# Kernel tuning notes

Measured on AMD Instinct MI355X. Metric: run time of the kernel, lower is better.

The kernel has to match this reference:

```python
import jax, jax.numpy as jnp
import numpy as np

N, E, IN, HID, HEADS, OUT = 50000, 800000, 2, 64, 4, 64


def setup_inputs() -> dict:
    key = jax.random.key(0)
    ks = jax.random.split(key, 16)
    g = lambda k, s: (jax.random.normal(k, s, dtype=jnp.float32) * 0.1)
    return {
        "x": jax.random.normal(ks[0], (N, IN), dtype=jnp.float32),
        # GraphConv(in->hid): lin_rel (with bias) on aggregated neighbors + lin_root on x
        "W_rel": g(ks[1], (IN, HID)), "b_rel": jnp.zeros((HID,), jnp.float32), "W_root": g(ks[2], (IN, HID)),
        # GATConv(hid -> hid, heads=4, concat)
        "W1": g(ks[3], (HID, HEADS * HID)), "a_src1": g(ks[4], (HEADS, HID)), "a_dst1": g(ks[5], (HEADS, HID)), "b1": jnp.zeros((HEADS * HID,), jnp.float32),
        # GATConv(hid*heads -> hid, heads=4, concat)
        "W2": g(ks[6], (HID * HEADS, HEADS * HID)), "a_src2": g(ks[7], (HEADS, HID)), "a_dst2": g(ks[8], (HEADS, HID)), "b2": jnp.zeros((HEADS * HID,), jnp.float32),
        # GATConv(hid*heads -> out, heads=1, concat=False)
        "W3": g(ks[9], (HID * HEADS, OUT)), "a_src3": g(ks[10], (1, OUT)), "a_dst3": g(ks[11], (1, OUT)), "b3": jnp.zeros((OUT,), jnp.float32),
        "edge_index": jax.random.randint(ks[12], (2, E), 0, N, dtype=jnp.int64),
    }


def graph_conv(x, src, dst, W_rel, b_rel, W_root, n):
    # out_i = (sum_{j->i} x_j) @ W_rel + b_rel + x_i @ W_root
    agg = jax.ops.segment_sum(x[src], dst, num_segments=n)
    return agg @ W_rel + b_rel + x @ W_root


def gat_conv(x, src, dst, W, a_s, a_d, b, heads, oc, concat):
    # src/dst already include self-loops (PyG add_self_loops=True default)
    n = x.shape[0]
    h = (x @ W).reshape(n, heads, oc)                      # [n, heads, oc]
    al_s = jnp.einsum("nhc,hc->nh", h, a_s)               # alpha_src per node
    al_d = jnp.einsum("nhc,hc->nh", h, a_d)               # alpha_dst per node
    e = jax.nn.leaky_relu(al_s[src] + al_d[dst], 0.2)     # [E, heads]
    m = jax.ops.segment_max(e, dst, num_segments=n)       # segment softmax (stable)
    w = jnp.exp(e - m[dst])
    den = jax.ops.segment_sum(w, dst, num_segments=n)
    alpha = w / (den[dst] + 1e-16)
    out = jax.ops.segment_sum(h[src] * alpha[..., None], dst, num_segments=n)
    out = out.reshape(n, heads * oc) if concat else out.mean(axis=1)
    return out + b


def reference(x, W_rel, b_rel, W_root, W1, a_src1, a_dst1, b1, W2, a_src2, a_dst2, b2, W3, a_src3, a_dst3, b3, edge_index):
    n = x.shape[0]
    src, dst = edge_index[0], edge_index[1]
    loop = jnp.arange(n, dtype=edge_index.dtype)
    src_sl = jnp.concatenate([src, loop])
    dst_sl = jnp.concatenate([dst, loop])
    h = jax.nn.relu(graph_conv(x, src, dst, W_rel, b_rel, W_root, n))
    h = jax.nn.relu(gat_conv(h, src_sl, dst_sl, W1, a_src1, a_dst1, b1, HEADS, HID, True))
    h = jax.nn.relu(gat_conv(h, src_sl, dst_sl, W2, a_src2, a_dst2, b2, HEADS, HID, True))
    return gat_conv(h, src_sl, dst_sl, W3, a_src3, a_dst3, b3, 1, OUT, False)
```

## Files before the change

### kernel.cpp

```cpp
#include <hip/hip_runtime.h>
#include <hip/hip_bf16.h>
#include <cstdint>


typedef __attribute__((ext_vector_type(8))) short bf16x8;
typedef __attribute__((ext_vector_type(4))) float f32x4;

__device__ inline unsigned short f2bf(float f) {
  union { float f; uint32_t u; } x; x.f = f;
  uint32_t r = x.u + 0x7FFF + ((x.u >> 16) & 1);
  return (unsigned short)(r >> 16);
}
__device__ inline float bf2f(unsigned short u) {
  union { uint32_t u; float f; } x; x.u = ((uint32_t)u) << 16; return x.f;
}
__device__ inline float lrelu02(float v) { return v > 0.f ? v : 0.2f * v; }

#define CHUNK 2048

__global__ __launch_bounds__(256) void bcount_kernel(const int* __restrict__ dst,
    int E, int N, int nbk, int* __restrict__ bcount) {
  __shared__ int lh[256];
  int t = threadIdx.x;
  lh[t] = 0;
  __syncthreads();
  int base = blockIdx.x * CHUNK;
  int lim = min(base + CHUNK, E + N);
  for (int i = base + t; i < lim; i += 256) {
    int d = (i < E) ? dst[i] : (i - E);
    atomicAdd(&lh[d >> 8], 1);
  }
  __syncthreads();
  if (t < nbk && lh[t]) atomicAdd(&bcount[t], lh[t]);
}

__global__ void bscan_kernel(const int* __restrict__ bcount, int nbk,
                             int* __restrict__ boffs, int* __restrict__ gcursor,
                             int* __restrict__ rowptr, int N, int total) {
  __shared__ int lds[256];
  int t = threadIdx.x;
  int v = (t < nbk) ? bcount[t] : 0;
  lds[t] = v;
  __syncthreads();
  for (int off = 1; off < 256; off <<= 1) {
    int x = lds[t];
    if (t >= off) x += lds[t - off];
    __syncthreads();
    lds[t] = x;
    __syncthreads();
  }
  if (t < nbk) {
    int ex = lds[t] - v;
    boffs[t] = ex;
    gcursor[t] = ex;
  }
  if (t == 0) {
    boffs[nbk] = total;
    rowptr[0] = 0;
    rowptr[N] = total;
  }
}

__global__ __launch_bounds__(256) void bscatter_kernel(const int* __restrict__ src,
    const int* __restrict__ dst, int E, int N, int nbk,
    int* __restrict__ gcursor, int2* __restrict__ pairs) {
  __shared__ int lh[256];
  __shared__ int gb[256];
  int t = threadIdx.x;
  lh[t] = 0;
  __syncthreads();
  int base = blockIdx.x * CHUNK;
  int lim = min(base + CHUNK, E + N);
  int myS[8], myD[8], myR[8];
#pragma unroll
  for (int u = 0; u < 8; ++u) {
    int i = base + t + u * 256;
    myD[u] = -1;
    if (i < lim) {
      int s, d;
      if (i < E) { s = src[i]; d = dst[i]; }
      else       { s = i - E; d = s; }
      myS[u] = s; myD[u] = d;
      myR[u] = atomicAdd(&lh[d >> 8], 1);
    }
  }
  __syncthreads();
  if (t < nbk && lh[t]) gb[t] = atomicAdd(&gcursor[t], lh[t]);
  __syncthreads();
#pragma unroll
  for (int u = 0; u < 8; ++u) {
    if (myD[u] >= 0) {
      int b = myD[u] >> 8;
      pairs[gb[b] + myR[u]] = make_int2(myS[u], myD[u]);
    }
  }
}

__global__ __launch_bounds__(256) void bcsr_kernel(const int2* __restrict__ pairs,
    const int* __restrict__ boffs, int nbk, int N,
    int* __restrict__ rowptr, int* __restrict__ adj) {
  __shared__ int lc[256];
  __shared__ int sc[256];
  int b = blockIdx.x;
  int t = threadIdx.x;
  int p0 = boffs[b], p1 = boffs[b + 1];
  lc[t] = 0;
  __syncthreads();
  for (int i = p0 + t; i < p1; i += 256)
    atomicAdd(&lc[pairs[i].y & 255], 1);
  __syncthreads();
  int v = lc[t];
  sc[t] = v;
  __syncthreads();
  for (int off = 1; off < 256; off <<= 1) {
    int x = sc[t];
    if (t >= off) x += sc[t - off];
    __syncthreads();
    sc[t] = x;
    __syncthreads();
  }
  int node = (b << 8) + t;
  if (node < N) rowptr[node + 1] = p0 + sc[t];
  lc[t] = p0 + sc[t] - v;
  __syncthreads();
  for (int i = p0 + t; i < p1; i += 256) {
    int2 pr = pairs[i];
    int slot = atomicAdd(&lc[pr.y & 255], 1);
    adj[slot] = pr.x;
  }
}

__global__ __launch_bounds__(256) void graphconv_csr(const float* __restrict__ x,
    const int* __restrict__ rowptr, const int* __restrict__ adj,
    const float* __restrict__ W_rel, const float* __restrict__ b_rel,
    const float* __restrict__ W_root, unsigned short* __restrict__ h0b, int N) {
  int w = threadIdx.x >> 6, l = threadIdx.x & 63;
  int node = blockIdx.x * 4 + w;
  if (node >= N) return;
  int s0 = rowptr[node], s1 = rowptr[node + 1];
  float a0 = 0.f, a1 = 0.f;
  for (int s = s0 + l; s < s1; s += 64) {
    int j = adj[s];
    float2 xv = *reinterpret_cast<const float2*>(x + (size_t)j * 2);
    a0 += xv.x; a1 += xv.y;
  }
#pragma unroll
  for (int off = 1; off < 64; off <<= 1) {
    a0 += __shfl_xor(a0, off);
    a1 += __shfl_xor(a1, off);
  }
  float2 xi = *reinterpret_cast<const float2*>(x + (size_t)node * 2);
  a0 -= xi.x; a1 -= xi.y;
  int c = l;
  float v = a0 * W_rel[c] + a1 * W_rel[64 + c]
          + xi.x * W_root[c] + xi.y * W_root[64 + c] + b_rel[c];
  h0b[(size_t)node * 64 + c] = f2bf(fmaxf(v, 0.f));
}

__global__ void wt3_kernel(const float* __restrict__ W1, unsigned short* __restrict__ Wt1,
                           const float* __restrict__ W2, unsigned short* __restrict__ Wt2,
                           const float* __restrict__ W3, unsigned short* __restrict__ Wt3) {
  int i = blockIdx.x * blockDim.x + threadIdx.x;
  if (i < 16384) {
    int n = i >> 6, k = i & 63;
    Wt1[i] = f2bf(W1[k * 256 + n]);
  } else if (i < 16384 + 65536) {
    int j = i - 16384;
    int n = j >> 8, k = j & 255;
    Wt2[j] = f2bf(W2[k * 256 + n]);
  } else if (i < 16384 + 65536 + 16384) {
    int j = i - 16384 - 65536;
    int n = j >> 8, k = j & 255;
    Wt3[j] = f2bf(W3[k * 64 + n]);
  }
}

template <int BM, int BN, int WARPS_M, int WARPS_N, int H>
__global__ __launch_bounds__(256) void mfma_gemm(const unsigned short* __restrict__ A,
    const unsigned short* __restrict__ Bt, unsigned short* __restrict__ C,
    const float* __restrict__ a_s, const float* __restrict__ a_d,
    float* __restrict__ alS, float* __restrict__ alD, int M, int N, int K) {
  __shared__ unsigned char lds[(BM + BN) * 80];
  unsigned char* As = lds;
  unsigned char* Bs = lds + BM * 80;
  int t = threadIdx.x;
  int w = t >> 6, l = t & 63;
  int wm = w / WARPS_N, wn = w % WARPS_N;
  int row0 = blockIdx.y * BM;
  int col0 = blockIdx.x * BN;
  f32x4 acc[4][4] = {};
  int slot = l >> 4, rr = l & 15;
  for (int k0 = 0; k0 < K; k0 += 32) {
    if (k0) __syncthreads();
#pragma unroll
    for (int u = 0; u < BM * 4 / 256; ++u) {
      int s = t + u * 256;
      int r = s >> 2, sl = s & 3;
      int gr = row0 + r;
      uint4 v = make_uint4(0u, 0u, 0u, 0u);
      if (gr < M) v = *reinterpret_cast<const uint4*>(A + (size_t)gr * K + k0 + sl * 8);
      *reinterpret_cast<uint4*>(As + r * 80 + sl * 16) = v;
    }
#pragma unroll
    for (int u = 0; u < BN * 4 / 256; ++u) {
      int s = t + u * 256;
      int r = s >> 2, sl = s & 3;
      uint4 v = *reinterpret_cast<const uint4*>(Bt + (size_t)(col0 + r) * K + k0 + sl * 8);
      *reinterpret_cast<uint4*>(Bs + r * 80 + sl * 16) = v;
    }
    __syncthreads();
    bf16x8 a[4], b[4];
#pragma unroll
    for (int i = 0; i < 4; ++i)
      a[i] = *reinterpret_cast<const bf16x8*>(As + (wm * 64 + i * 16 + rr) * 80 + slot * 16);
#pragma unroll
    for (int j = 0; j < 4; ++j)
      b[j] = *reinterpret_cast<const bf16x8*>(Bs + (wn * 64 + j * 16 + rr) * 80 + slot * 16);
#pragma unroll
    for (int i = 0; i < 4; ++i)
#pragma unroll
      for (int j = 0; j < 4; ++j)
        acc[i][j] = __builtin_amdgcn_mfma_f32_16x16x32_bf16(a[i], b[j], acc[i][j], 0, 0, 0);
  }
  int rb = row0 + wm * 64 + (l >> 4) * 4;
  int cb = col0 + wn * 64 + (l & 15);
#pragma unroll
  for (int i = 0; i < 4; ++i) {
#pragma unroll
    for (int r = 0; r < 4; ++r) {
      int gr = rb + i * 16 + r;
      if (gr < M) {
#pragma unroll
        for (int j = 0; j < 4; ++j)
          C[(size_t)gr * N + cb + j * 16] = f2bf(acc[i][j][r]);
      }
    }
  }
  int hd = (col0 >> 6) + wn;
  int ch = l & 15;
  float as0 = a_s[hd * 64 + ch], as1 = a_s[hd * 64 + ch + 16];
  float as2 = a_s[hd * 64 + ch + 32], as3 = a_s[hd * 64 + ch + 48];
  float ad0 = a_d[hd * 64 + ch], ad1 = a_d[hd * 64 + ch + 16];
  float ad2 = a_d[hd * 64 + ch + 32], ad3 = a_d[hd * 64 + ch + 48];
#pragma unroll
  for (int i = 0; i < 4; ++i) {
#pragma unroll
    for (int r = 0; r < 4; ++r) {
      float ps = acc[i][0][r] * as0 + acc[i][1][r] * as1
               + acc[i][2][r] * as2 + acc[i][3][r] * as3;
      float pd = acc[i][0][r] * ad0 + acc[i][1][r] * ad1
               + acc[i][2][r] * ad2 + acc[i][3][r] * ad3;
#pragma unroll
      for (int off = 1; off < 16; off <<= 1) {
        ps += __shfl_xor(ps, off);
        pd += __shfl_xor(pd, off);
      }
      if ((l & 15) == 0) {
        int gr = rb + i * 16 + r;
        if (gr < M) {
          alS[gr * H + hd] = ps;
          alD[gr * H + hd] = pd;
        }
      }
    }
  }
}

template <bool RELU>
__global__ __launch_bounds__(256) void gat_gather256(const unsigned short* __restrict__ hW,
    const float* __restrict__ alS, const float* __restrict__ alD,
    const int* __restrict__ rowptr, const int* __restrict__ adj,
    const float* __restrict__ bias, unsigned short* __restrict__ outb, int N) {
  int w = threadIdx.x >> 6, l = threadIdx.x & 63;
  int node = blockIdx.x * 4 + w;
  if (node >= N) return;
  int head = l >> 4;
  int c = l << 2;
  float ald = alD[node * 4 + head];
  int s0 = rowptr[node], s1 = rowptr[node + 1];
  float den = 0.f, a0 = 0.f, a1 = 0.f, a2 = 0.f, a3 = 0.f;
  int s = s0;
  for (; s + 8 <= s1; s += 8) {
    int ix[8];
#pragma unroll
    for (int u = 0; u < 8; ++u) ix[u] = adj[s + u];
    float vv[8];
#pragma unroll
    for (int u = 0; u < 8; ++u) vv[u] = alS[ix[u] * 4 + head];
    ushort4 hh[8];
#pragma unroll
    for (int u = 0; u < 8; ++u)
      hh[u] = *reinterpret_cast<const ushort4*>(hW + (size_t)ix[u] * 256 + c);
    float wt[8];
#pragma unroll
    for (int u = 0; u < 8; ++u) wt[u] = __expf(lrelu02(vv[u] + ald));
#pragma unroll
    for (int u = 0; u < 8; ++u) {
      den += wt[u];
      a0 += wt[u] * bf2f(hh[u].x);
      a1 += wt[u] * bf2f(hh[u].y);
      a2 += wt[u] * bf2f(hh[u].z);
      a3 += wt[u] * bf2f(hh[u].w);
    }
  }
  for (; s + 4 <= s1; s += 4) {
    int i0 = adj[s + 0], i1 = adj[s + 1], i2 = adj[s + 2], i3 = adj[s + 3];
    float v0 = alS[i0 * 4 + head];
    float v1 = alS[i1 * 4 + head];
    float v2 = alS[i2 * 4 + head];
    float v3 = alS[i3 * 4 + head];
    ushort4 h0 = *reinterpret_cast<const ushort4*>(hW + (size_t)i0 * 256 + c);
    ushort4 h1 = *reinterpret_cast<const ushort4*>(hW + (size_t)i1 * 256 + c);
    ushort4 h2 = *reinterpret_cast<const ushort4*>(hW + (size_t)i2 * 256 + c);
    ushort4 h3 = *reinterpret_cast<const ushort4*>(hW + (size_t)i3 * 256 + c);
    float w0 = __expf(lrelu02(v0 + ald));
    float w1 = __expf(lrelu02(v1 + ald));
    float w2 = __expf(lrelu02(v2 + ald));
    float w3 = __expf(lrelu02(v3 + ald));
    den += (w0 + w1) + (w2 + w3);
    a0 += w0 * bf2f(h0.x) + w1 * bf2f(h1.x) + w2 * bf2f(h2.x) + w3 * bf2f(h3.x);
    a1 += w0 * bf2f(h0.y) + w1 * bf2f(h1.y) + w2 * bf2f(h2.y) + w3 * bf2f(h3.y);
    a2 += w0 * bf2f(h0.z) + w1 * bf2f(h1.z) + w2 * bf2f(h2.z) + w3 * bf2f(h3.z);
    a3 += w0 * bf2f(h0.w) + w1 * bf2f(h1.w) + w2 * bf2f(h2.w) + w3 * bf2f(h3.w);
  }
  for (; s < s1; ++s) {
    int i0 = adj[s];
    float v0 = alS[i0 * 4 + head];
    ushort4 h0 = *reinterpret_cast<const ushort4*>(hW + (size_t)i0 * 256 + c);
    float w0 = __expf(lrelu02(v0 + ald));
    den += w0;
    a0 += w0 * bf2f(h0.x);
    a1 += w0 * bf2f(h0.y);
    a2 += w0 * bf2f(h0.z);
    a3 += w0 * bf2f(h0.w);
  }
  float inv = 1.f / (den + 1e-16f);
  float o0 = a0 * inv + bias[c + 0];
  float o1 = a1 * inv + bias[c + 1];
  float o2 = a2 * inv + bias[c + 2];
  float o3 = a3 * inv + bias[c + 3];
  if (RELU) {
    o0 = fmaxf(o0, 0.f); o1 = fmaxf(o1, 0.f);
    o2 = fmaxf(o2, 0.f); o3 = fmaxf(o3, 0.f);
  }
  ushort4 ov;
  ov.x = f2bf(o0); ov.y = f2bf(o1); ov.z = f2bf(o2); ov.w = f2bf(o3);
  *reinterpret_cast<ushort4*>(outb + (size_t)node * 256 + c) = ov;
}

template <bool RELU>
__global__ __launch_bounds__(256) void gat_gather64(const unsigned short* __restrict__ hW,
    const float* __restrict__ alS, const float* __restrict__ alD,
    const int* __restrict__ rowptr, const int* __restrict__ adj,
    const float* __restrict__ bias, float* __restrict__ out, int N) {
  int w = threadIdx.x >> 6, l = threadIdx.x & 63;
  int node = blockIdx.x * 4 + w;
  if (node >= N) return;
  int g = l >> 4;
  int c = (l & 15) << 2;
  float ald = alD[node];
  int s0 = rowptr[node], s1 = rowptr[node + 1];
  float den = 0.f, a0 = 0.f, a1 = 0.f, a2 = 0.f, a3 = 0.f;
  int s = s0 + g;
  for (; s + 12 < s1; s += 16) {
    int ix[4];
    ix[0] = adj[s]; ix[1] = adj[s + 4]; ix[2] = adj[s + 8]; ix[3] = adj[s + 12];
    float vv[4];
#pragma unroll
    for (int u = 0; u < 4; ++u) vv[u] = alS[ix[u]];
    ushort4 hh[4];
#pragma unroll
    for (int u = 0; u < 4; ++u)
      hh[u] = *reinterpret_cast<const ushort4*>(hW + (size_t)ix[u] * 64 + c);
#pragma unroll
    for (int u = 0; u < 4; ++u) {
      float wt = __expf(lrelu02(vv[u] + ald));
      den += wt;
      a0 += wt * bf2f(hh[u].x);
      a1 += wt * bf2f(hh[u].y);
      a2 += wt * bf2f(hh[u].z);
      a3 += wt * bf2f(hh[u].w);
    }
  }
  for (; s < s1; s += 4) {
    int i0 = adj[s];
    float v0 = alS[i0];
    ushort4 h0 = *reinterpret_cast<const ushort4*>(hW + (size_t)i0 * 64 + c);
    float w0 = __expf(lrelu02(v0 + ald));
    den += w0;
    a0 += w0 * bf2f(h0.x);
    a1 += w0 * bf2f(h0.y);
    a2 += w0 * bf2f(h0.z);
    a3 += w0 * bf2f(h0.w);
  }
#pragma unroll
  for (int off = 16; off <= 32; off <<= 1) {
    den += __shfl_xor(den, off);
    a0 += __shfl_xor(a0, off);
    a1 += __shfl_xor(a1, off);
    a2 += __shfl_xor(a2, off);
    a3 += __shfl_xor(a3, off);
  }
  if (g == 0) {
    float inv = 1.f / (den + 1e-16f);
    float o0 = a0 * inv + bias[c + 0];
    float o1 = a1 * inv + bias[c + 1];
    float o2 = a2 * inv + bias[c + 2];
    float o3 = a3 * inv + bias[c + 3];
    if (RELU) {
      o0 = fmaxf(o0, 0.f); o1 = fmaxf(o1, 0.f);
      o2 = fmaxf(o2, 0.f); o3 = fmaxf(o3, 0.f);
    }
    *reinterpret_cast<float4*>(out + (size_t)node * 64 + c) = make_float4(o0, o1, o2, o3);
  }
}

extern "C" void kernel_launch(void* const* d_in, const int* in_sizes, int n_in,
                              void* d_out, int out_size, void* d_ws, size_t ws_size,
                              hipStream_t stream) {
  const float* x      = (const float*)d_in[0];
  const float* W_rel  = (const float*)d_in[1];
  const float* b_rel  = (const float*)d_in[2];
  const float* W_root = (const float*)d_in[3];
  const float* W1     = (const float*)d_in[4];
  const float* a_s1   = (const float*)d_in[5];
  const float* a_d1   = (const float*)d_in[6];
  const float* b1     = (const float*)d_in[7];
  const float* W2     = (const float*)d_in[8];
  const float* a_s2   = (const float*)d_in[9];
  const float* a_d2   = (const float*)d_in[10];
  const float* b2     = (const float*)d_in[11];
  const float* W3     = (const float*)d_in[12];
  const float* a_s3   = (const float*)d_in[13];
  const float* a_d3   = (const float*)d_in[14];
  const float* b3     = (const float*)d_in[15];
  const int*   ei     = (const int*)d_in[16];

  int N = in_sizes[0] / 2;
  int E = in_sizes[16] / 2;
  const int* srcp = ei;
  const int* dstp = ei + E;
  int ESL = E + N;
  int nbk = (N + 255) >> 8;

  unsigned short* h0b  = (unsigned short*)d_ws;
  unsigned short* bufX = h0b + (size_t)N * 64;
  unsigned short* bufY = bufX + (size_t)N * 256;
  unsigned short* bufZ = bufY + (size_t)N * 256;
  unsigned short* Wt1  = bufZ + (size_t)N * 64;
  unsigned short* Wt2  = Wt1 + 256 * 64;
  unsigned short* Wt3  = Wt2 + 256 * 256;
  float* alS  = (float*)(Wt3 + 64 * 256);
  float* alD  = alS + (size_t)N * 4;
  int2* pairs = (int2*)(alD + (size_t)N * 4);
  int* adj    = (int*)(pairs + ESL);
  int* rowptr = adj + ESL;
  int* bcount = rowptr + (N + 1);
  int* boffs  = bcount + 256;
  int* gcursor= boffs + 257;

  hipMemsetAsync(bcount, 0, 256 * sizeof(int), stream);

  int tb = 256;
  int nch = (ESL + CHUNK - 1) / CHUNK;
  int gN4 = (N + 3) / 4;

  bcount_kernel<<<nch, tb, 0, stream>>>(dstp, E, N, nbk, bcount);
  bscan_kernel<<<1, 256, 0, stream>>>(bcount, nbk, boffs, gcursor, rowptr, N, ESL);
  bscatter_kernel<<<nch, tb, 0, stream>>>(srcp, dstp, E, N, nbk, gcursor, pairs);
  bcsr_kernel<<<nbk, tb, 0, stream>>>(pairs, boffs, nbk, N, rowptr, adj);

  wt3_kernel<<<(98304 + tb - 1) / tb, tb, 0, stream>>>(W1, Wt1, W2, Wt2, W3, Wt3);

  graphconv_csr<<<gN4, 256, 0, stream>>>(x, rowptr, adj, W_rel, b_rel, W_root, h0b, N);

  dim3 gA(256 / 128, (N + 127) / 128);
  dim3 gB(1, (N + 255) / 256);

  mfma_gemm<128, 128, 2, 2, 4><<<gA, 256, 0, stream>>>(h0b, Wt1, bufX, a_s1, a_d1, alS, alD, N, 256, 64);
  gat_gather256<true><<<gN4, 256, 0, stream>>>(bufX, alS, alD, rowptr, adj, b1, bufY, N);

  mfma_gemm<128, 128, 2, 2, 4><<<gA, 256, 0, stream>>>(bufY, Wt2, bufX, a_s2, a_d2, alS, alD, N, 256, 256);
  gat_gather256<true><<<gN4, 256, 0, stream>>>(bufX, alS, alD, rowptr, adj, b2, bufY, N);

  mfma_gemm<256, 64, 4, 1, 1><<<gB, 256, 0, stream>>>(bufY, Wt3, bufZ, a_s3, a_d3, alS, alD, N, 64, 256);
  gat_gather64<false><<<gN4, 256, 0, stream>>>(bufZ, alS, alD, rowptr, adj, b3, (float*)d_out, N);
}
```

Measured before the change: 294.8 us.

## Precompute per-edge attention weights and gather 256-wide features by column slices

Splits each 256-wide GAT aggregation into two kernels. The first computes exp(leaky_relu) attention weights per edge and head once, stored as bf16 planes. The second is a sliced gather where each block handles a 32-column slice for 16 nodes, with 8 lanes per edge-slot reducing through shuffles. The slicing is meant to improve cache locality of the feature gathers and spread edges across more lanes. The cost is an extra kernel launch, an extra E-sized write and read, and bf16 rounding of the attention weights.

```diff
diff --git a/kernel.cpp b/kernel.cpp
--- a/kernel.cpp
+++ b/kernel.cpp
@@ -266,86 +266,80 @@
   }
 }
 
-template <bool RELU>
-__global__ __launch_bounds__(256) void gat_gather256(const unsigned short* __restrict__ hW,
-    const float* __restrict__ alS, const float* __restrict__ alD,
-    const int* __restrict__ rowptr, const int* __restrict__ adj,
-    const float* __restrict__ bias, unsigned short* __restrict__ outb, int N) {
+__global__ __launch_bounds__(256) void edgew4_kernel(const float4* __restrict__ alS4,
+    const float4* __restrict__ alD4, const int* __restrict__ rowptr,
+    const int* __restrict__ adj, unsigned short* __restrict__ wexpH,
+    int N, int ESL) {
   int w = threadIdx.x >> 6, l = threadIdx.x & 63;
   int node = blockIdx.x * 4 + w;
   if (node >= N) return;
-  int head = l >> 4;
-  int c = l << 2;
-  float ald = alD[node * 4 + head];
+  float4 ad = alD4[node];
   int s0 = rowptr[node], s1 = rowptr[node + 1];
-  float den = 0.f, a0 = 0.f, a1 = 0.f, a2 = 0.f, a3 = 0.f;
-  int s = s0;
-  for (; s + 8 <= s1; s += 8) {
-    int ix[8];
-#pragma unroll
-    for (int u = 0; u < 8; ++u) ix[u] = adj[s + u];
-    float vv[8];
-#pragma unroll
-    for (int u = 0; u < 8; ++u) vv[u] = alS[ix[u] * 4 + head];
-    ushort4 hh[8];
-#pragma unroll
-    for (int u = 0; u < 8; ++u)
-      hh[u] = *reinterpret_cast<const ushort4*>(hW + (size_t)ix[u] * 256 + c);
-    float wt[8];
-#pragma unroll
-    for (int u = 0; u < 8; ++u) wt[u] = __expf(lrelu02(vv[u] + ald));
-#pragma unroll
-    for (int u = 0; u < 8; ++u) {
-      den += wt[u];
-      a0 += wt[u] * bf2f(hh[u].x);
-      a1 += wt[u] * bf2f(hh[u].y);
-      a2 += wt[u] * bf2f(hh[u].z);
-      a3 += wt[u] * bf2f(hh[u].w);
-    }
-  }
-  for (; s + 4 <= s1; s += 4) {
-    int i0 = adj[s + 0], i1 = adj[s + 1], i2 = adj[s + 2], i3 = adj[s + 3];
-    float v0 = alS[i0 * 4 + head];
-    float v1 = alS[i1 * 4 + head];
-    float v2 = alS[i2 * 4 + head];
-    float v3 = alS[i3 * 4 + head];
-    ushort4 h0 = *reinterpret_cast<const ushort4*>(hW + (size_t)i0 * 256 + c);
-    ushort4 h1 = *reinterpret_cast<const ushort4*>(hW + (size_t)i1 * 256 + c);
-    ushort4 h2 = *reinterpret_cast<const ushort4*>(hW + (size_t)i2 * 256 + c);
-    ushort4 h3 = *reinterpret_cast<const ushort4*>(hW + (size_t)i3 * 256 + c);
-    float w0 = __expf(lrelu02(v0 + ald));
-    float w1 = __expf(lrelu02(v1 + ald));
-    float w2 = __expf(lrelu02(v2 + ald));
-    float w3 = __expf(lrelu02(v3 + ald));
-    den += (w0 + w1) + (w2 + w3);
-    a0 += w0 * bf2f(h0.x) + w1 * bf2f(h1.x) + w2 * bf2f(h2.x) + w3 * bf2f(h3.x);
-    a1 += w0 * bf2f(h0.y) + w1 * bf2f(h1.y) + w2 * bf2f(h2.y) + w3 * bf2f(h3.y);
-    a2 += w0 * bf2f(h0.z) + w1 * bf2f(h1.z) + w2 * bf2f(h2.z) + w3 * bf2f(h3.z);
-    a3 += w0 * bf2f(h0.w) + w1 * bf2f(h1.w) + w2 * bf2f(h2.w) + w3 * bf2f(h3.w);
-  }
-  for (; s < s1; ++s) {
-    int i0 = adj[s];
-    float v0 = alS[i0 * 4 + head];
-    ushort4 h0 = *reinterpret_cast<const ushort4*>(hW + (size_t)i0 * 256 + c);
-    float w0 = __expf(lrelu02(v0 + ald));
-    den += w0;
-    a0 += w0 * bf2f(h0.x);
-    a1 += w0 * bf2f(h0.y);
-    a2 += w0 * bf2f(h0.z);
-    a3 += w0 * bf2f(h0.w);
-  }
-  float inv = 1.f / (den + 1e-16f);
-  float o0 = a0 * inv + bias[c + 0];
-  float o1 = a1 * inv + bias[c + 1];
-  float o2 = a2 * inv + bias[c + 2];
-  float o3 = a3 * inv + bias[c + 3];
-  if (RELU) {
-    o0 = fmaxf(o0, 0.f); o1 = fmaxf(o1, 0.f);
-    o2 = fmaxf(o2, 0.f); o3 = fmaxf(o3, 0.f);
-  }
-  ushort4 ov;
-  ov.x = f2bf(o0); ov.y = f2bf(o1); ov.z = f2bf(o2); ov.w = f2bf(o3);
-  *reinterpret_cast<ushort4*>(outb + (size_t)node * 256 + c) = ov;
+  for (int s = s0 + l; s < s1; s += 64) {
+    int j = adj[s];
+    float4 as = alS4[j];
+    wexpH[0 * (size_t)ESL + s] = f2bf(__expf(lrelu02(as.x + ad.x)));
+    wexpH[1 * (size_t)ESL + s] = f2bf(__expf(lrelu02(as.y + ad.y)));
+    wexpH[2 * (size_t)ESL + s] = f2bf(__expf(lrelu02(as.z + ad.z)));
+    wexpH[3 * (size_t)ESL + s] = f2bf(__expf(lrelu02(as.w + ad.w)));
+  }
+}
+
+template <bool RELU>
+__global__ __launch_bounds__(256) void gat_g256s(const unsigned short* __restrict__ hW,
+    const unsigned short* __restrict__ wexpH,
+    const int* __restrict__ rowptr, const int* __restrict__ adj,
+    const float* __restrict__ bias, unsigned short* __restrict__ outb,
+    int N, int ESL) {
+  int slice = blockIdx.x & 7;
+  int ng = blockIdx.x >> 3;
+  int w = threadIdx.x >> 6, l = threadIdx.x & 63;
+  int slot = l >> 3;
+  int q = l & 7;
+  int cbase = slice * 32 + q * 4;
+  const unsigned short* wplane = wexpH + (size_t)(slice >> 1) * ESL;
+  float b0 = bias[cbase + 0], b1 = bias[cbase + 1];
+  float b2 = bias[cbase + 2], b3 = bias[cbase + 3];
+#pragma unroll
+  for (int k = 0; k < 4; ++k) {
+    int node = ng * 16 + w * 4 + k;
+    if (node < N) {
+      int s0 = rowptr[node], s1 = rowptr[node + 1];
+      float den = 0.f, a0 = 0.f, a1 = 0.f, a2 = 0.f, a3 = 0.f;
+      for (int e = s0 + slot; e < s1; e += 8) {
+        int idx = adj[e];
+        float wt = bf2f(wplane[e]);
+        ushort4 hv = *reinterpret_cast<const ushort4*>(hW + (size_t)idx * 256 + cbase);
+        den += wt;
+        a0 += wt * bf2f(hv.x);
+        a1 += wt * bf2f(hv.y);
+        a2 += wt * bf2f(hv.z);
+        a3 += wt * bf2f(hv.w);
+      }
+#pragma unroll
+      for (int off = 8; off <= 32; off <<= 1) {
+        den += __shfl_xor(den, off);
+        a0 += __shfl_xor(a0, off);
+        a1 += __shfl_xor(a1, off);
+        a2 += __shfl_xor(a2, off);
+        a3 += __shfl_xor(a3, off);
+      }
+      if (slot == 0) {
+        float inv = 1.f / (den + 1e-16f);
+        float o0 = a0 * inv + b0;
+        float o1 = a1 * inv + b1;
+        float o2 = a2 * inv + b2;
+        float o3 = a3 * inv + b3;
+        if (RELU) {
+          o0 = fmaxf(o0, 0.f); o1 = fmaxf(o1, 0.f);
+          o2 = fmaxf(o2, 0.f); o3 = fmaxf(o3, 0.f);
+        }
+        ushort4 ov;
+        ov.x = f2bf(o0); ov.y = f2bf(o1); ov.z = f2bf(o2); ov.w = f2bf(o3);
+        *reinterpret_cast<ushort4*>(outb + (size_t)node * 256 + cbase) = ov;
+      }
+    }
+  }
 }
 
 template <bool RELU>
@@ -443,14 +437,15 @@
   int ESL = E + N;
   int nbk = (N + 255) >> 8;
 
-  unsigned short* h0b  = (unsigned short*)d_ws;
-  unsigned short* bufX = h0b + (size_t)N * 64;
-  unsigned short* bufY = bufX + (size_t)N * 256;
-  unsigned short* bufZ = bufY + (size_t)N * 256;
-  unsigned short* Wt1  = bufZ + (size_t)N * 64;
-  unsigned short* Wt2  = Wt1 + 256 * 64;
-  unsigned short* Wt3  = Wt2 + 256 * 256;
-  float* alS  = (float*)(Wt3 + 64 * 256);
+  unsigned short* h0b   = (unsigned short*)d_ws;
+  unsigned short* bufX  = h0b + (size_t)N * 64;
+  unsigned short* bufY  = bufX + (size_t)N * 256;
+  unsigned short* bufZ  = bufY + (size_t)N * 256;
+  unsigned short* Wt1   = bufZ + (size_t)N * 64;
+  unsigned short* Wt2   = Wt1 + 256 * 64;
+  unsigned short* Wt3   = Wt2 + 256 * 256;
+  unsigned short* wexpH = Wt3 + 64 * 256;
+  float* alS  = (float*)(wexpH + (size_t)4 * ESL);
   float* alD  = alS + (size_t)N * 4;
   int2* pairs = (int2*)(alD + (size_t)N * 4);
   int* adj    = (int*)(pairs + ESL);
@@ -464,6 +459,7 @@
   int tb = 256;
   int nch = (ESL + CHUNK - 1) / CHUNK;
   int gN4 = (N + 3) / 4;
+  int gSl = 8 * ((N + 15) / 16);
 
   bcount_kernel<<<nch, tb, 0, stream>>>(dstp, E, N, nbk, bcount);
   bscan_kernel<<<1, 256, 0, stream>>>(bcount, nbk, boffs, gcursor, rowptr, N, ESL);
@@ -478,10 +474,12 @@
   dim3 gB(1, (N + 255) / 256);
 
   mfma_gemm<128, 128, 2, 2, 4><<<gA, 256, 0, stream>>>(h0b, Wt1, bufX, a_s1, a_d1, alS, alD, N, 256, 64);
-  gat_gather256<true><<<gN4, 256, 0, stream>>>(bufX, alS, alD, rowptr, adj, b1, bufY, N);
+  edgew4_kernel<<<gN4, 256, 0, stream>>>((const float4*)alS, (const float4*)alD, rowptr, adj, wexpH, N, ESL);
+  gat_g256s<true><<<gSl, 256, 0, stream>>>(bufX, wexpH, rowptr, adj, b1, bufY, N, ESL);
 
   mfma_gemm<128, 128, 2, 2, 4><<<gA, 256, 0, stream>>>(bufY, Wt2, bufX, a_s2, a_d2, alS, alD, N, 256, 256);
-  gat_gather256<true><<<gN4, 256, 0, stream>>>(bufX, alS, alD, rowptr, adj, b2, bufY, N);
+  edgew4_kernel<<<gN4, 256, 0, stream>>>((const float4*)alS, (const float4*)alD, rowptr, adj, wexpH, N, ESL);
+  gat_g256s<true><<<gSl, 256, 0, stream>>>(bufX, wexpH, rowptr, adj, b2, bufY, N, ESL);
 
   mfma_gemm<256, 64, 4, 1, 1><<<gB, 256, 0, stream>>>(bufY, Wt3, bufZ, a_s3, a_d3, alS, alD, N, 64, 256);
   gat_gather64<false><<<gN4, 256, 0, stream>>>(bufZ, alS, alD, rowptr, adj, b3, (float*)d_out, N);
```

Measured after the change: 453.7 us. 1.54x slower.
